# Kernel tuning notes

Hardware: AMD Instinct MI355X
Metric: run time of the kernel (lower is better)

The kernel has to match this reference:

```python
import jax, jax.numpy as jnp
import numpy as np

HID = 3584      # hidden_size
NQ = 16         # num query heads
NKV = 8         # num kv heads
D = 256         # head_dim
SCALE = 256.0 ** -0.5   # query_pre_attn_scalar ** -0.5
CAP = 50.0      # attn_logits_soft_cap
WINDOW = 2048   # interleaved sliding window (even layer)
THETA = 10000.0
B, S = 1, 4096


def _rope(x, positions):
    """Neox-style RoPE. x: [B,S,N,D], positions: [B,S] int."""
    half = D // 2
    inv_freq = 1.0 / (THETA ** (jnp.arange(half, dtype=jnp.float32) / half))
    freqs = positions.astype(jnp.float32)[:, :, None] * inv_freq  # [B,S,half]
    cos = jnp.cos(freqs)[:, :, None, :]  # [B,S,1,half]
    sin = jnp.sin(freqs)[:, :, None, :]
    x1, x2 = x[..., :half], x[..., half:]
    return jnp.concatenate([x1 * cos - x2 * sin, x2 * cos + x1 * sin], axis=-1)


def setup_inputs() -> dict:
    key = jax.random.key(0)
    k1, k2, k3 = jax.random.split(key, 3)
    positions = jnp.broadcast_to(jnp.arange(S, dtype=jnp.int64)[None, :], (B, S))
    hidden_states = jax.random.normal(k1, (B, S, HID), dtype=jnp.float32)
    # scale weights ~ 1/sqrt(fan_in) so activations are O(1)
    w_qkv = jax.random.normal(k2, ((NQ + 2 * NKV) * D, HID), dtype=jnp.float32) * (HID ** -0.5)
    w_o = jax.random.normal(k3, (HID, NQ * D), dtype=jnp.float32) * ((NQ * D) ** -0.5)
    return {"positions": positions, "hidden_states": hidden_states, "w_qkv": w_qkv, "w_o": w_o}


def reference(positions, hidden_states, w_qkv, w_o):
    q_size, kv_size = NQ * D, NKV * D
    qkv = jnp.einsum('bsh,oh->bso', hidden_states, w_qkv)
    q = qkv[..., :q_size].reshape(B, S, NQ, D)
    k = qkv[..., q_size:q_size + kv_size].reshape(B, S, NKV, D)
    v = qkv[..., q_size + kv_size:].reshape(B, S, NKV, D)
    q = _rope(q, positions)
    k = _rope(k, positions)
    # GQA: repeat kv heads to match query heads
    g = NQ // NKV
    k = jnp.repeat(k, g, axis=2)  # [B,S,NQ,D]
    v = jnp.repeat(v, g, axis=2)
    scores = jnp.einsum('bqhd,bkhd->bhqk', q, k) * SCALE
    # Gemma2 logit soft-capping
    scores = CAP * jnp.tanh(scores / CAP)
    i = jnp.arange(S)[:, None]
    j = jnp.arange(S)[None, :]
    mask = (j <= i) & (i - j < WINDOW)  # causal + sliding window
    scores = jnp.where(mask, scores, -1e30)
    probs = jax.nn.softmax(scores, axis=-1)
    attn = jnp.einsum('bhqk,bkhd->bqhd', probs, v).reshape(B, S, NQ * D)
    return jnp.einsum('bso,ho->bsh', attn, w_o)
```

## Files before the change

kernel.cpp:

```cpp
#include <hip/hip_runtime.h>
#include <hip/hip_bf16.h>

typedef __bf16 bf16_t;
typedef __bf16 bf16x4 __attribute__((ext_vector_type(4)));
typedef __bf16 bf16x8 __attribute__((ext_vector_type(8)));
typedef float f32x4 __attribute__((ext_vector_type(4)));

#define HIDDEN 3584
#define NQH 16
#define NKVH 8
#define DH 256
#define SEQ 4096
#define QKV_COLS 8192
#define Q_SIZE 4096
#define KV_SIZE 2048
#define WINDOW 2048
#define SCALE_F 0.0625f
#define CAP_F 50.0f

__device__ __forceinline__ void gload16(const bf16_t* g, bf16_t* l) {
  __builtin_amdgcn_global_load_lds((__attribute__((address_space(1))) void*)g,
                                   (__attribute__((address_space(3))) void*)l, 16, 0, 0);
}

__global__ __launch_bounds__(256) void cvt_f32_to_bf16(const float* __restrict__ src,
                                                       bf16_t* __restrict__ dst, long n8) {
  long i = (long)blockIdx.x * 256 + threadIdx.x;
  if (i >= n8) return;
  const float4* s4 = (const float4*)src;
  float4 a = s4[i * 2];
  float4 b = s4[i * 2 + 1];
  bf16x8 o;
  o[0] = (bf16_t)a.x; o[1] = (bf16_t)a.y; o[2] = (bf16_t)a.z; o[3] = (bf16_t)a.w;
  o[4] = (bf16_t)b.x; o[5] = (bf16_t)b.y; o[6] = (bf16_t)b.z; o[7] = (bf16_t)b.w;
  *(bf16x8*)(dst + i * 8) = o;
}

#define TILE(T, WSTR, STAGE)                                                                \
  {                                                                                         \
    char* buf = lds + ((T) & 3) * 32768;                                                    \
    bf16x8 af[8], b0, b1, b2, b3;                                                           \
    _Pragma("unroll")                                                                       \
    for (int i = 0; i < 8; ++i) af[i] = *(const bf16x8*)(buf + aoff + i * 1024);            \
    b0 = *(const bf16x8*)(buf + boff);                                                      \
    b1 = *(const bf16x8*)(buf + boff + 1024);                                               \
    if (STAGE) {                                                                            \
      char* d = lds + (((T) + 3) & 3) * 32768;                                              \
      gload16(sA0 + ((T) + 3) * 32, (bf16_t*)(d + sdst0));                                  \
      gload16(sA1 + ((T) + 3) * 32, (bf16_t*)(d + 8192 + sdst0));                           \
    }                                                                                       \
    __builtin_amdgcn_s_setprio(1);                                                          \
    _Pragma("unroll")                                                                       \
    for (int i = 0; i < 8; ++i) {                                                           \
      acc[i][0] = __builtin_amdgcn_mfma_f32_16x16x32_bf16(af[i], b0, acc[i][0], 0, 0, 0);   \
      acc[i][1] = __builtin_amdgcn_mfma_f32_16x16x32_bf16(af[i], b1, acc[i][1], 0, 0, 0);   \
    }                                                                                       \
    __builtin_amdgcn_s_setprio(0);                                                          \
    __builtin_amdgcn_s_barrier();                                                           \
    b2 = *(const bf16x8*)(buf + boff + 2048);                                               \
    b3 = *(const bf16x8*)(buf + boff + 3072);                                               \
    if (STAGE) {                                                                            \
      char* d = lds + (((T) + 3) & 3) * 32768;                                              \
      gload16(sB0 + ((T) + 3) * 32, (bf16_t*)(d + 16384 + sdst0));                          \
      gload16(sB1 + ((T) + 3) * 32, (bf16_t*)(d + 24576 + sdst0));                          \
    }                                                                                       \
    __builtin_amdgcn_s_setprio(1);                                                          \
    _Pragma("unroll")                                                                       \
    for (int i = 0; i < 8; ++i) {                                                           \
      acc[i][2] = __builtin_amdgcn_mfma_f32_16x16x32_bf16(af[i], b2, acc[i][2], 0, 0, 0);   \
      acc[i][3] = __builtin_amdgcn_mfma_f32_16x16x32_bf16(af[i], b3, acc[i][3], 0, 0, 0);   \
    }                                                                                       \
    __builtin_amdgcn_s_setprio(0);                                                          \
    asm volatile("s_waitcnt vmcnt(" WSTR ")" ::: "memory");                                 \
    __builtin_amdgcn_s_barrier();                                                           \
  }

template <int K, int MODE>
__global__ __launch_bounds__(512, 2) void gemm_bt(const bf16_t* __restrict__ A,
                                                  const bf16_t* __restrict__ B,
                                                  void* __restrict__ Cout,
                                                  bf16_t* __restrict__ vtout, int N) {
  constexpr int NT = K / 32;
  __shared__ char lds[4 * 32768];
  int tid = threadIdx.x;
  int lane = tid & 63, w = tid >> 6;
  int wm = w >> 2, wn = w & 3;
  int r16 = lane & 15, g = lane >> 4;
  int bid = blockIdx.x;
  long bm = (long)((bid & 7) * 2 + ((bid >> 3) & 1)) * 256;
  long bn = (long)(bid >> 4) * 256;
  int ro = r16 >> 1;
  int asl = ((g + ((r16 & 1) << 2)) ^ ro) << 4;
  int aoff = wm * 8192 + ro * 128 + asl;
  int boff = 16384 + wn * 4096 + ro * 128 + asl;
  int slr = lane >> 3;
  int lc = (lane & 7) ^ slr;
  int kc8 = (lc & 3) * 8;
  long mr0 = (long)(w * 8 + slr) * 2 + (lc >> 2);
  long mr1 = mr0 + 128;
  const bf16_t* sA0 = A + (bm + mr0) * K + kc8;
  const bf16_t* sA1 = A + (bm + mr1) * K + kc8;
  const bf16_t* sB0 = B + (bn + mr0) * K + kc8;
  const bf16_t* sB1 = B + (bn + mr1) * K + kc8;
  int sdst0 = w * 1024;
  f32x4 acc[8][4] = {};
#pragma unroll
  for (int u = 0; u < 3; ++u) {
    char* d = lds + u * 32768;
    gload16(sA0 + u * 32, (bf16_t*)(d + sdst0));
    gload16(sA1 + u * 32, (bf16_t*)(d + 8192 + sdst0));
    gload16(sB0 + u * 32, (bf16_t*)(d + 16384 + sdst0));
    gload16(sB1 + u * 32, (bf16_t*)(d + 24576 + sdst0));
  }
  asm volatile("s_waitcnt vmcnt(8)" ::: "memory");
  __builtin_amdgcn_s_barrier();
  int t = 0;
  for (; t < NT - 3; ++t) TILE(t, "8", true);
  TILE(t, "4", false); ++t;
  TILE(t, "0", false); ++t;
  TILE(t, "0", false);
  if (MODE == 1 && bn >= (Q_SIZE + KV_SIZE)) {
#pragma unroll
    for (int i = 0; i < 8; ++i) {
      long row = bm + wm * 128 + i * 16 + g * 4;
#pragma unroll
      for (int j = 0; j < 4; ++j) {
        long colv = bn - (Q_SIZE + KV_SIZE) + wn * 64 + j * 16 + r16;
        bf16x4 o;
#pragma unroll
        for (int r = 0; r < 4; ++r) o[r] = (bf16_t)acc[i][j][r];
        *(bf16x4*)&vtout[colv * SEQ + row] = o;
      }
    }
  } else {
#pragma unroll
    for (int i = 0; i < 8; ++i)
#pragma unroll
      for (int j = 0; j < 4; ++j)
#pragma unroll
        for (int r = 0; r < 4; ++r) {
          long row = bm + wm * 128 + i * 16 + g * 4 + r;
          long col = bn + wn * 64 + j * 16 + r16;
          if (MODE == 1) ((bf16_t*)Cout)[row * N + col] = (bf16_t)acc[i][j][r];
          else           ((float*)Cout)[row * N + col]  = acc[i][j][r];
        }
  }
}

__global__ __launch_bounds__(256) void rope_k_kernel(bf16_t* __restrict__ qkv) {
  long idx = (long)blockIdx.x * 256 + threadIdx.x;
  int i8 = (int)(idx & 15) * 8;
  long rem = idx >> 4;
  int head = (int)(rem & 7);
  int s = (int)(rem >> 3);
  long p1 = (long)s * QKV_COLS + Q_SIZE + head * DH + i8;
  bf16x8 x1 = *(const bf16x8*)&qkv[p1];
  bf16x8 x2 = *(const bf16x8*)&qkv[p1 + 128];
  bf16x8 o1, o2;
#pragma unroll
  for (int j = 0; j < 8; ++j) {
    float inv_freq = exp2f((float)(i8 + j) * -0.10381025296522976f);
    float fr = (float)s * inv_freq;
    float sn, cs;
    sincosf(fr, &sn, &cs);
    float a = (float)x1[j], b = (float)x2[j];
    o1[j] = (bf16_t)(a * cs - b * sn);
    o2[j] = (bf16_t)(b * cs + a * sn);
  }
  *(bf16x8*)&qkv[p1] = o1;
  *(bf16x8*)&qkv[p1 + 128] = o2;
}

__global__ __launch_bounds__(512, 2) void attn_kernel(const bf16_t* __restrict__ qkv,
                                                      const bf16_t* __restrict__ vt,
                                                      bf16_t* __restrict__ attn_out) {
  __shared__ bf16_t Kb[2][64 * 256];
  __shared__ bf16_t Vb[2][256 * 64];
  __shared__ bf16_t Pl[8 * 1024];
  int tid = threadIdx.x;
  int lane = tid & 63, w = tid >> 6;
  int r16 = lane & 15, g = lane >> 4;
  int bid = blockIdx.x;
  int swz = (bid & 7) * 64 + (bid >> 3);
  int h = swz >> 5;
  int qb0 = swz & 31;
  int qb = (h & 1) ? (31 - qb0) : qb0;
  int kvh = h >> 1;
  int qw = qb * 128 + w * 16;
  bf16x8 qf[8];
  long qoff = (long)(qw + r16) * QKV_COLS + h * DH + g * 8;
#pragma unroll
  for (int kk = 0; kk < 8; ++kk) qf[kk] = *(const bf16x8*)&qkv[qoff + kk * 32];
#pragma unroll
  for (int kk = 0; kk < 4; ++kk)
#pragma unroll
    for (int j = 0; j < 8; ++j) {
      int d = kk * 32 + g * 8 + j;
      float inv_freq = exp2f((float)d * -0.10381025296522976f);
      float fr = (float)(qw + r16) * inv_freq;
      float sn, cs;
      sincosf(fr, &sn, &cs);
      float a = (float)qf[kk][j], b2 = (float)qf[kk + 4][j];
      qf[kk][j] = (bf16_t)(a * cs - b2 * sn);
      qf[kk + 4][j] = (bf16_t)(b2 * cs + a * sn);
    }
  f32x4 acc[16] = {};
  float lsum[4] = {};
  const bf16_t* kg = qkv + Q_SIZE + (long)kvh * DH;
  const bf16_t* vg = vt + (long)kvh * DH * SEQ;
  bf16_t* pw = Pl + w * 1024;
  int lo = qb * 128 - (WINDOW - 1);
  int t0 = lo > 0 ? (lo >> 6) : 0;
  int t1 = qb * 2 + 2;
  int qlo = qw, qhi = qw + 15;

#define ATTN_STAGE(TT)                                                                   \
  {                                                                                      \
    int b_ = (TT) & 1;                                                                   \
    int kb_ = (TT) * 64;                                                                 \
    _Pragma("unroll")                                                                    \
    for (int c = 0; c < 4; ++c) {                                                        \
      int rowk = w * 8 + c * 2 + (lane >> 5);                                            \
      gload16(kg + (long)(kb_ + rowk) * QKV_COLS + (((lane & 31) ^ (rowk & 7)) * 8),     \
              &Kb[b_][w * 2048 + c * 512]);                                              \
      int rowv = w * 32 + c * 8 + (lane >> 3);                                           \
      gload16(vg + (long)rowv * SEQ + kb_ + (((lane & 7) ^ (rowv & 7)) * 8),             \
              &Vb[b_][w * 2048 + c * 512]);                                              \
    }                                                                                    \
  }

  ATTN_STAGE(t0);
  __syncthreads();
  for (int tt = t0; tt < t1; ++tt) {
    if (tt + 1 < t1) ATTN_STAGE(tt + 1);
    int b = tt & 1;
    int kb = tt * 64;
    bool active = !(kb > qhi || kb + 63 < qlo - (WINDOW - 1));
    if (active) {
      bool full = (kb + 63 <= qlo) && (qhi - kb <= WINDOW - 1);
      f32x4 sc[4] = {};
      __builtin_amdgcn_s_setprio(1);
#pragma unroll
      for (int kk = 0; kk < 8; ++kk) {
        int sl = ((kk * 4 + g) ^ (r16 & 7)) * 8;
#pragma unroll
        for (int c = 0; c < 4; ++c) {
          bf16x8 kf = *(const bf16x8*)&Kb[b][(c * 16 + r16) * 256 + sl];
          sc[c] = __builtin_amdgcn_mfma_f32_16x16x32_bf16(qf[kk], kf, sc[c], 0, 0, 0);
        }
      }
      __builtin_amdgcn_s_setprio(0);
#pragma unroll
      for (int c = 0; c < 4; ++c)
#pragma unroll
        for (int r = 0; r < 4; ++r) {
          float s = sc[c][r];
          float e = __expf(s * (2.0f * SCALE_F / CAP_F));
          float rr = __builtin_amdgcn_rcpf(e + 1.0f);
          float p = __expf(fmaf(-100.0f, rr, 38.0f));
          if (!full) {
            int q = qw + g * 4 + r;
            int k = kb + c * 16 + r16;
            p = ((k <= q) && (q - k < WINDOW)) ? p : 0.0f;
          }
          lsum[r] += p;
          int prow = g * 4 + r;
          int pbyte = prow * 128 + ((c * 32 + r16 * 2) ^ ((prow & 7) << 4));
          *(bf16_t*)((char*)pw + pbyte) = (bf16_t)p;
        }
      bf16x8 pa[2];
#pragma unroll
      for (int pk = 0; pk < 2; ++pk) {
        int pb = r16 * 128 + ((pk * 64 + g * 16) ^ ((r16 & 7) << 4));
        pa[pk] = *(const bf16x8*)((const char*)pw + pb);
      }
      __builtin_amdgcn_s_setprio(1);
#pragma unroll
      for (int dt = 0; dt < 16; ++dt) {
        int vrow = (dt * 16 + r16) * 64;
        bf16x8 vf0 = *(const bf16x8*)&Vb[b][vrow + ((g ^ (r16 & 7)) * 8)];
        acc[dt] = __builtin_amdgcn_mfma_f32_16x16x32_bf16(pa[0], vf0, acc[dt], 0, 0, 0);
        bf16x8 vf1 = *(const bf16x8*)&Vb[b][vrow + (((4 + g) ^ (r16 & 7)) * 8)];
        acc[dt] = __builtin_amdgcn_mfma_f32_16x16x32_bf16(pa[1], vf1, acc[dt], 0, 0, 0);
      }
      __builtin_amdgcn_s_setprio(0);
    }
    __syncthreads();
  }
  float inv[4];
#pragma unroll
  for (int r = 0; r < 4; ++r) {
    float s = lsum[r];
    s += __shfl_xor(s, 1);
    s += __shfl_xor(s, 2);
    s += __shfl_xor(s, 4);
    s += __shfl_xor(s, 8);
    inv[r] = 1.0f / s;
  }
#pragma unroll
  for (int dt = 0; dt < 16; ++dt)
#pragma unroll
    for (int r = 0; r < 4; ++r) {
      long row = qw + g * 4 + r;
      attn_out[row * Q_SIZE + h * DH + dt * 16 + r16] = (bf16_t)(acc[dt][r] * inv[r]);
    }
}

extern "C" void kernel_launch(void* const* d_in, const int* in_sizes, int n_in,
                              void* d_out, int out_size, void* d_ws, size_t ws_size,
                              hipStream_t stream) {
  const float* hid_f  = (const float*)d_in[1];
  const float* wqkv_f = (const float*)d_in[2];
  const float* wo_f   = (const float*)d_in[3];
  float* out = (float*)d_out;
  char* ws = (char*)d_ws;
  bf16_t* qkv    = (bf16_t*)(ws);
  bf16_t* wo_b   = (bf16_t*)(ws + 67108864);
  bf16_t* hid_b  = (bf16_t*)(ws + 96468992);
  bf16_t* wqkv_b = (bf16_t*)(ws + 125829120);
  bf16_t* attn_b = (bf16_t*)(ws + 96468992);
  bf16_t* vt     = (bf16_t*)d_out;

  cvt_f32_to_bf16<<<7168, 256, 0, stream>>>(hid_f, hid_b, 14680064 / 8);
  cvt_f32_to_bf16<<<14336, 256, 0, stream>>>(wqkv_f, wqkv_b, 29360128 / 8);
  cvt_f32_to_bf16<<<7168, 256, 0, stream>>>(wo_f, wo_b, 14680064 / 8);
  gemm_bt<HIDDEN, 1><<<512, 512, 0, stream>>>(hid_b, wqkv_b, qkv, vt, QKV_COLS);
  rope_k_kernel<<<2048, 256, 0, stream>>>(qkv);
  attn_kernel<<<512, 512, 0, stream>>>(qkv, vt, attn_b);
  gemm_bt<Q_SIZE, 0><<<224, 512, 0, stream>>>(attn_b, wo_b, out, nullptr, HIDDEN);
}
```

Before: 576.9 us.

## Fuse K RoPE into QKV GEMM epilogue and merge conversion kernels

Applies RoPE to the K columns inside the QKV GEMM epilogue. Each wave exchanges its bf16 accumulator tile through LDS with the partner wave holding the other half of the head dimension, which removes the separate rope_k kernel and its read/write pass over K. The three fp32-to-bf16 conversion launches are also merged into one kernel with range-based dispatch, saving launch overhead. In exchange the epilogue gains an LDS round trip, a barrier and sincos work, and the partner half is rounded to bf16 before rotation, as in the original.

```diff
diff --git a/kernel.cpp b/kernel.cpp
--- a/kernel.cpp
+++ b/kernel.cpp
@@ -23,17 +23,26 @@
                                    (__attribute__((address_space(3))) void*)l, 16, 0, 0);
 }
 
-__global__ __launch_bounds__(256) void cvt_f32_to_bf16(const float* __restrict__ src,
-                                                       bf16_t* __restrict__ dst, long n8) {
+__global__ __launch_bounds__(256) void cvt_all(const float* __restrict__ hid,
+                                               const float* __restrict__ wqkv,
+                                               const float* __restrict__ wo,
+                                               bf16_t* __restrict__ hb,
+                                               bf16_t* __restrict__ qb,
+                                               bf16_t* __restrict__ wb) {
   long i = (long)blockIdx.x * 256 + threadIdx.x;
-  if (i >= n8) return;
+  const float* src;
+  bf16_t* dst;
+  long off;
+  if (i < 1835008)       { src = hid;  dst = hb; off = i; }
+  else if (i < 5505024)  { src = wqkv; dst = qb; off = i - 1835008; }
+  else                   { src = wo;   dst = wb; off = i - 5505024; }
   const float4* s4 = (const float4*)src;
-  float4 a = s4[i * 2];
-  float4 b = s4[i * 2 + 1];
+  float4 a = s4[off * 2];
+  float4 b = s4[off * 2 + 1];
   bf16x8 o;
   o[0] = (bf16_t)a.x; o[1] = (bf16_t)a.y; o[2] = (bf16_t)a.z; o[3] = (bf16_t)a.w;
   o[4] = (bf16_t)b.x; o[5] = (bf16_t)b.y; o[6] = (bf16_t)b.z; o[7] = (bf16_t)b.w;
-  *(bf16x8*)(dst + i * 8) = o;
+  *(bf16x8*)(dst + off * 8) = o;
 }
 
 #define TILE(T, WSTR, STAGE)                                                                \
@@ -132,6 +141,41 @@
         *(bf16x4*)&vtout[colv * SEQ + row] = o;
       }
     }
+  } else if (MODE == 1 && bn >= Q_SIZE) {
+#pragma unroll
+    for (int i = 0; i < 8; ++i)
+#pragma unroll
+      for (int j = 0; j < 4; ++j) {
+        bf16x4 o;
+#pragma unroll
+        for (int r = 0; r < 4; ++r) o[r] = (bf16_t)acc[i][j][r];
+        *(bf16x4*)(lds + w * 16384 + i * 2048 + j * 512 + lane * 8) = o;
+      }
+    __syncthreads();
+    int pw = w ^ 2;
+    bool hi = (wn & 2) != 0;
+    float invf[4];
+#pragma unroll
+    for (int j = 0; j < 4; ++j) {
+      int ih = (wn & 1) * 64 + j * 16 + r16;
+      invf[j] = exp2f((float)ih * -0.10381025296522976f);
+    }
+#pragma unroll
+    for (int i = 0; i < 8; ++i)
+#pragma unroll
+      for (int j = 0; j < 4; ++j) {
+        bf16x4 part = *(const bf16x4*)(lds + pw * 16384 + i * 2048 + j * 512 + lane * 8);
+#pragma unroll
+        for (int r = 0; r < 4; ++r) {
+          long row = bm + wm * 128 + i * 16 + g * 4 + r;
+          float fr = (float)row * invf[j];
+          float sn, cs;
+          sincosf(fr, &sn, &cs);
+          float own = acc[i][j][r], pt = (float)part[r];
+          float o = hi ? (own * cs + pt * sn) : (own * cs - pt * sn);
+          ((bf16_t*)Cout)[row * QKV_COLS + bn + wn * 64 + j * 16 + r16] = (bf16_t)o;
+        }
+      }
   } else {
 #pragma unroll
     for (int i = 0; i < 8; ++i)
@@ -145,30 +189,6 @@
           else           ((float*)Cout)[row * N + col]  = acc[i][j][r];
         }
   }
-}
-
-__global__ __launch_bounds__(256) void rope_k_kernel(bf16_t* __restrict__ qkv) {
-  long idx = (long)blockIdx.x * 256 + threadIdx.x;
-  int i8 = (int)(idx & 15) * 8;
-  long rem = idx >> 4;
-  int head = (int)(rem & 7);
-  int s = (int)(rem >> 3);
-  long p1 = (long)s * QKV_COLS + Q_SIZE + head * DH + i8;
-  bf16x8 x1 = *(const bf16x8*)&qkv[p1];
-  bf16x8 x2 = *(const bf16x8*)&qkv[p1 + 128];
-  bf16x8 o1, o2;
-#pragma unroll
-  for (int j = 0; j < 8; ++j) {
-    float inv_freq = exp2f((float)(i8 + j) * -0.10381025296522976f);
-    float fr = (float)s * inv_freq;
-    float sn, cs;
-    sincosf(fr, &sn, &cs);
-    float a = (float)x1[j], b = (float)x2[j];
-    o1[j] = (bf16_t)(a * cs - b * sn);
-    o2[j] = (bf16_t)(b * cs + a * sn);
-  }
-  *(bf16x8*)&qkv[p1] = o1;
-  *(bf16x8*)&qkv[p1 + 128] = o2;
 }
 
 __global__ __launch_bounds__(512, 2) void attn_kernel(const bf16_t* __restrict__ qkv,
@@ -321,11 +341,8 @@
   bf16_t* attn_b = (bf16_t*)(ws + 96468992);
   bf16_t* vt     = (bf16_t*)d_out;
 
-  cvt_f32_to_bf16<<<7168, 256, 0, stream>>>(hid_f, hid_b, 14680064 / 8);
-  cvt_f32_to_bf16<<<14336, 256, 0, stream>>>(wqkv_f, wqkv_b, 29360128 / 8);
-  cvt_f32_to_bf16<<<7168, 256, 0, stream>>>(wo_f, wo_b, 14680064 / 8);
+  cvt_all<<<28672, 256, 0, stream>>>(hid_f, wqkv_f, wo_f, hid_b, wqkv_b, wo_b);
   gemm_bt<HIDDEN, 1><<<512, 512, 0, stream>>>(hid_b, wqkv_b, qkv, vt, QKV_COLS);
-  rope_k_kernel<<<2048, 256, 0, stream>>>(qkv);
   attn_kernel<<<512, 512, 0, stream>>>(qkv, vt, attn_b);
   gemm_bt<Q_SIZE, 0><<<224, 512, 0, stream>>>(attn_b, wo_b, out, nullptr, HIDDEN);
 }
```

Result: slower. 686.4 us (+19.0%).
